# Kernel optimization log

Hardware: AMD Instinct MI355X
Metric: run time of the kernel (lower is better)

The kernel has to match this reference:

```python
import jax, jax.numpy as jnp
import numpy as np

E, L, S, C, H, NEXP = 1024, 25, 64, 128, 512, 8  # edges, sh coeffs, grid pts, dim_in, 4*dim_in, experts


def _ln(x, g, b, eps=1e-5):
    m = jnp.mean(x, axis=-1, keepdims=True)
    v = jnp.mean((x - m) ** 2, axis=-1, keepdims=True)
    return (x - m) * jax.lax.rsqrt(v + eps) * g + b


def setup_inputs() -> dict:
    key = jax.random.key(0)
    ks = jax.random.split(key, 20)
    rn = lambda k, shp: jax.random.normal(k, shp, jnp.float32) * 0.05
    return {
        "message": jax.random.normal(ks[0], (E, L, C), jnp.float32),
        "gate_output": jax.nn.softmax(jax.random.normal(ks[1], (E, NEXP), jnp.float32), axis=-1),
        "batch": jnp.sort(jax.random.randint(ks[2], (E,), 0, 64)),
        "ln1_g": jnp.ones((C,), jnp.float32), "ln1_b": jnp.zeros((C,), jnp.float32),
        "wq": rn(ks[3], (C, C)), "bq": jnp.zeros((C,), jnp.float32),
        "wk": rn(ks[4], (C, C)), "bk": jnp.zeros((C,), jnp.float32),
        "wv": rn(ks[5], (C, C)), "bv": jnp.zeros((C,), jnp.float32),
        "norm_l0_g": jnp.ones((C,), jnp.float32), "norm_l0_b": jnp.zeros((C,), jnp.float32),
        "fc_l0_w": rn(ks[6], (C, C)), "fc_l0_b": jnp.zeros((C,), jnp.float32),
        "exp_ln_g": jnp.ones((NEXP, C), jnp.float32), "exp_ln_b": jnp.zeros((NEXP, C), jnp.float32),
        "exp_w1": rn(ks[7], (NEXP, C, H)), "exp_b1": jnp.zeros((NEXP, H), jnp.float32),
        "exp_w2": rn(ks[8], (NEXP, H, C)), "exp_b2": jnp.zeros((NEXP, C), jnp.float32),
        "to_grid_mat": rn(ks[9], (S, L)),
        "from_grid_mat": rn(ks[10], (L, S)),
        "pos_emb": jax.random.normal(ks[11], (S, 3), jnp.float32),
    }


def reference(message, gate_output, batch, ln1_g, ln1_b, wq, bq, wk, bk, wv, bv,
              norm_l0_g, norm_l0_b, fc_l0_w, fc_l0_b,
              exp_ln_g, exp_ln_b, exp_w1, exp_b1, exp_w2, exp_b2,
              to_grid_mat, from_grid_mat, pos_emb):
    # l=0 scalar branch: LN -> Linear -> SiLU on the first SH coefficient
    msg_l0 = jax.nn.silu(_ln(message[:, 0:1, :], norm_l0_g, norm_l0_b) @ fc_l0_w + fc_l0_b)  # [E,1,C]
    # SH coeffs -> spherical grid (eval mode: no random rotation)
    g = jnp.einsum('sl,elc->esc', to_grid_mat, message)  # [E,S,C]
    m = _ln(g, ln1_g, ln1_b)
    q = m @ wq + bq
    k = m @ wk + bk
    v = m @ wv + bv
    # spherical RoE: concat grid xyz positions to q and k
    pe = jnp.broadcast_to(pos_emb[None].astype(q.dtype), (q.shape[0],) + pos_emb.shape)  # [E,S,3]
    q = jnp.concatenate([q, pe], axis=-1)  # [E,S,C+3]
    k = jnp.concatenate([k, pe], axis=-1)
    scale = 1.0 / jnp.sqrt(jnp.asarray(q.shape[-1], q.dtype))
    attn = jax.nn.softmax(jnp.einsum('esc,etc->est', q, k) * scale, axis=-1)
    out = jnp.einsum('est,etc->esc', attn, v)  # [E,S,C]
    # gate-weighted dense sum over experts (LN -> Linear -> SiLU -> Linear)
    acc = jnp.zeros_like(out)
    for i in range(NEXP):
        h = _ln(out, exp_ln_g[i], exp_ln_b[i])
        h = jax.nn.silu(h @ exp_w1[i] + exp_b1[i]) @ exp_w2[i] + exp_b2[i]
        acc = acc + h * gate_output[:, i][:, None, None]
    # grid -> SH coeffs, then splice in the l0 branch
    fro = jnp.einsum('ls,esc->elc', from_grid_mat, acc)  # [E,L,C]
    return jnp.concatenate([msg_l0, fro[:, 1:, :]], axis=1)
```

## Files before the change

### kernel.cpp

```cpp
#include <hip/hip_runtime.h>
#include <hip/hip_bf16.h>

#define E_ 1024
#define L_ 25
#define S_ 64
#define C_ 128
#define H_ 512
#define NEXP_ 8

#define OFF_W     0
#define OFF_PEDOT 128
#define OFF_B1P   4224
#define OFF_GTF   8320
#define OFF_WVTF  16512
#define OFF_TGF   24704
#define OFF_G     25728
#define OFF_W1S   42112
#define OFF_W2S   304256
#define OFF_NOUT  566400

typedef float floatx4 __attribute__((ext_vector_type(4)));
typedef __bf16 bf16x8 __attribute__((ext_vector_type(8)));
typedef __bf16 bf16x4 __attribute__((ext_vector_type(4)));

__global__ void prep1(const float* __restrict__ wq, const float* __restrict__ bq,
                      const float* __restrict__ wk, const float* __restrict__ bk,
                      const float* __restrict__ pe, float* __restrict__ ws) {
    int b = blockIdx.x, tid = threadIdx.x;
    (void)bk;
    if (b < 64) {
        int a = b * 2 + (tid >> 7);
        int col = tid & 127;
        const float* ra = wq + a * C_;
        const float* rb = wk + col * C_;
        float acc = 0.f;
        for (int c = 0; c < C_; ++c) acc += ra[c] * rb[c];
        ws[OFF_G + a * C_ + col] = acc;
    } else {
        if (tid < 128) {
            float acc = 0.f; const float* r = wk + tid * C_;
            for (int c = 0; c < C_; ++c) acc += r[c] * bq[c];
            ws[OFF_W + tid] = acc;
        }
        for (int idx = tid; idx < 64 * 64; idx += 256) {
            int s = idx >> 6, t = idx & 63;
            ws[OFF_PEDOT + idx] = pe[s*3]*pe[t*3] + pe[s*3+1]*pe[t*3+1] + pe[s*3+2]*pe[t*3+2];
        }
    }
}

__global__ void prep2(const float* __restrict__ elnb, const float* __restrict__ w1,
                      const float* __restrict__ b1, float* __restrict__ ws) {
    __shared__ float red[256];
    int b = blockIdx.x;
    int i = b >> 3, seg = b & 7;
    int hl = threadIdx.x & 63, part = threadIdx.x >> 6;
    int h = seg * 64 + hl;
    const float* wcol = w1 + i * 65536 + h;
    float acc = 0.f;
    for (int c = part * 32; c < part * 32 + 32; ++c)
        acc += elnb[i * 128 + c] * wcol[c * 512];
    red[threadIdx.x] = acc;
    __syncthreads();
    if (part == 0)
        ws[OFF_B1P + i * 512 + h] = red[hl] + red[hl + 64] + red[hl + 128] + red[hl + 192]
                                  + b1[i * 512 + h];
}

__global__ void prepSwz(const float* __restrict__ elng, const float* __restrict__ w1,
                        const float* __restrict__ w2,
                        __hip_bfloat16* __restrict__ w1s, __hip_bfloat16* __restrict__ w2s) {
    int idx = blockIdx.x * 256 + threadIdx.x;
    if (idx < 524288) {
        int f = idx >> 9, r = idx & 511;
        int lane = r >> 3, j = r & 7;
        int kt = f & 3, htg = (f >> 2) & 31, ex = f >> 7;
        int c = kt * 32 + (lane >> 4) * 8 + j;
        int h = htg * 16 + (lane & 15);
        w1s[idx] = __float2bfloat16(elng[ex * 128 + c] * w1[ex * 65536 + c * 512 + h]);
    } else {
        int i2 = idx - 524288;
        int f = i2 >> 9, r = i2 & 511;
        int lane = r >> 3, j = r & 7;
        int ktg = f & 15, ctg = (f >> 4) & 7, ex = f >> 7;
        int h = ktg * 32 + (lane >> 4) * 8 + j;
        int c = ctg * 16 + (lane & 15);
        w2s[i2] = __float2bfloat16(w2[ex * 65536 + h * 128 + c]);
    }
}

__global__ void prepSwzA(const float* __restrict__ ws, const float* __restrict__ wv,
                         const float* __restrict__ tg,
                         __hip_bfloat16* __restrict__ gtf, __hip_bfloat16* __restrict__ wvtf,
                         __hip_bfloat16* __restrict__ tgf) {
    int idx = blockIdx.x * 256 + threadIdx.x;
    if (idx < 32768) {
        int i2 = idx & 16383;
        int f = i2 >> 9, r = i2 & 511;
        int lane = r >> 3, j = r & 7;
        int kt = f & 3, Nt = f >> 2;
        int k = kt * 32 + (lane >> 4) * 8 + j;
        int n = Nt * 16 + (lane & 15);
        if (idx < 16384) {
            gtf[i2] = __float2bfloat16(ws[OFF_G + k * 128 + n]);
        } else {
            wvtf[i2] = __float2bfloat16(wv[k * 128 + n]);
        }
    } else {
        int i3 = idx - 32768;
        int f = i3 >> 9, r = i3 & 511;
        int lane = r >> 3, j = r & 7;
        int m = f * 16 + (lane & 15);
        int k = (lane >> 4) * 8 + j;
        tgf[i3] = (k < 25) ? __float2bfloat16(tg[m * 25 + k]) : __float2bfloat16(0.f);
    }
}

__global__ __launch_bounds__(256) void kernA(
        const float* __restrict__ message, const float* __restrict__ ln1g,
        const float* __restrict__ ln1b, const float* __restrict__ bv,
        const float* __restrict__ ws_ro,
        const __hip_bfloat16* __restrict__ gtf, const __hip_bfloat16* __restrict__ wvtf,
        const __hip_bfloat16* __restrict__ tgf,
        __hip_bfloat16* __restrict__ nout) {
    __shared__ __align__(16) char sA[64 * 272];
    __shared__ __align__(16) char sB[64 * 272];
    __shared__ __align__(16) char sC[128 * 144];
    __shared__ __align__(16) float sStP[512];
    __shared__ __align__(16) float sSt2[128];
    __shared__ float sMw[64];

    const int e = blockIdx.x, tid = threadIdx.x;
    const int w = tid >> 6, lane = tid & 63, quad = lane >> 4, col = lane & 15;

    float* sMsgF = (float*)sB;
    for (int i = tid; i < 3200; i += 256) sMsgF[i] = message[(size_t)e * 3200 + i];
    __syncthreads();

    char* sMt = sC;
    for (int i = tid; i < 4096; i += 256) {
        int c = i >> 5, l = i & 31;
        float v = (l < 25) ? sMsgF[l * 128 + c] : 0.f;
        *(__hip_bfloat16*)(sMt + c * 80 + l * 2) = __float2bfloat16(v);
    }
    __syncthreads();

    floatx4 accG[4][2];
    {
        #pragma unroll
        for (int mt = 0; mt < 4; ++mt) { accG[mt][0] = (floatx4)0.f; accG[mt][1] = (floatx4)0.f; }
        bf16x8 a[4], b[2];
        #pragma unroll
        for (int mt = 0; mt < 4; ++mt) a[mt] = *(const bf16x8*)(tgf + mt * 512 + lane * 8);
        #pragma unroll
        for (int nt = 0; nt < 2; ++nt)
            b[nt] = *(const bf16x8*)(sMt + ((2 * w + nt) * 16 + col) * 80 + quad * 16);
        #pragma unroll
        for (int mt = 0; mt < 4; ++mt)
            #pragma unroll
            for (int nt = 0; nt < 2; ++nt)
                accG[mt][nt] = __builtin_amdgcn_mfma_f32_16x16x32_bf16(a[mt], b[nt], accG[mt][nt], 0, 0, 0);
    }
    #pragma unroll
    for (int mt = 0; mt < 4; ++mt)
        #pragma unroll
        for (int reg = 0; reg < 4; ++reg) {
            float v0 = accG[mt][0][reg], v1 = accG[mt][1][reg];
            float sm = v0 + v1, sq = v0 * v0 + v1 * v1;
            #pragma unroll
            for (int m = 1; m < 16; m <<= 1) {
                sm += __shfl_xor(sm, m, 64);
                sq += __shfl_xor(sq, m, 64);
            }
            if (col == 0) {
                int s = mt * 16 + quad * 4 + reg;
                sStP[(s * 4 + w) * 2]     = sm;
                sStP[(s * 4 + w) * 2 + 1] = sq;
            }
        }
    __syncthreads();
    if (tid < 64) {
        float sm = 0.f, sq = 0.f;
        #pragma unroll
        for (int k = 0; k < 4; ++k) {
            sm += sStP[(tid * 4 + k) * 2];
            sq += sStP[(tid * 4 + k) * 2 + 1];
        }
        float mean = sm * (1.f / 128.f);
        float rstd = rsqrtf(sq * (1.f / 128.f) - mean * mean + 1e-5f);
        sSt2[tid * 2] = mean; sSt2[tid * 2 + 1] = rstd;
    }
    __syncthreads();
    {
        float g1[2], b1v[2];
        #pragma unroll
        for (int nt = 0; nt < 2; ++nt) {
            int c = (2 * w + nt) * 16 + col;
            g1[nt] = ln1g[c]; b1v[nt] = ln1b[c];
        }
        #pragma unroll
        for (int mt = 0; mt < 4; ++mt)
            #pragma unroll
            for (int reg = 0; reg < 4; ++reg) {
                int s = mt * 16 + quad * 4 + reg;
                float mean = sSt2[s * 2], rstd = sSt2[s * 2 + 1];
                #pragma unroll
                for (int nt = 0; nt < 2; ++nt) {
                    int c = (2 * w + nt) * 16 + col;
                    ((__hip_bfloat16*)(sA + s * 272))[c] =
                        __float2bfloat16((accG[mt][nt][reg] - mean) * rstd * g1[nt] + b1v[nt]);
                }
            }
    }
    __syncthreads();

    {
        int t = tid >> 2, part = tid & 3;
        const __hip_bfloat16* mr = (const __hip_bfloat16*)(sA + t * 272) + part * 32;
        const float* wv_ = ws_ro + OFF_W + part * 32;
        float acc = 0.f;
        #pragma unroll
        for (int k = 0; k < 32; ++k) acc += __bfloat162float(mr[k]) * wv_[k];
        acc += __shfl_xor(acc, 1, 64);
        acc += __shfl_xor(acc, 2, 64);
        if (part == 0) sMw[t] = acc;
    }

    {
        floatx4 accZ[4][2];
        #pragma unroll
        for (int mt = 0; mt < 4; ++mt) { accZ[mt][0] = (floatx4)0.f; accZ[mt][1] = (floatx4)0.f; }
        #pragma unroll
        for (int kt = 0; kt < 4; ++kt) {
            bf16x8 a[4], b[2];
            #pragma unroll
            for (int mt = 0; mt < 4; ++mt)
                a[mt] = *(const bf16x8*)(sA + (mt * 16 + col) * 272 + kt * 64 + quad * 16);
            #pragma unroll
            for (int nt = 0; nt < 2; ++nt)
                b[nt] = *(const bf16x8*)(gtf + ((2 * w + nt) * 4 + kt) * 512 + lane * 8);
            #pragma unroll
            for (int mt = 0; mt < 4; ++mt)
                #pragma unroll
                for (int nt = 0; nt < 2; ++nt)
                    accZ[mt][nt] = __builtin_amdgcn_mfma_f32_16x16x32_bf16(a[mt], b[nt], accZ[mt][nt], 0, 0, 0);
        }
        #pragma unroll
        for (int mt = 0; mt < 4; ++mt)
            #pragma unroll
            for (int nt = 0; nt < 2; ++nt) {
                int j = (2 * w + nt) * 16 + col;
                #pragma unroll
                for (int reg = 0; reg < 4; ++reg)
                    ((__hip_bfloat16*)(sB + (mt * 16 + quad * 4 + reg) * 272))[j] =
                        __float2bfloat16(accZ[mt][nt][reg]);
            }
    }
    __syncthreads();

    {
        floatx4 accS[4];
        #pragma unroll
        for (int mt = 0; mt < 4; ++mt) accS[mt] = (floatx4)0.f;
        #pragma unroll
        for (int kt = 0; kt < 4; ++kt) {
            bf16x8 a[4];
            #pragma unroll
            for (int mt = 0; mt < 4; ++mt)
                a[mt] = *(const bf16x8*)(sB + (mt * 16 + col) * 272 + kt * 64 + quad * 16);
            bf16x8 b = *(const bf16x8*)(sA + (w * 16 + col) * 272 + kt * 64 + quad * 16);
            #pragma unroll
            for (int mt = 0; mt < 4; ++mt)
                accS[mt] = __builtin_amdgcn_mfma_f32_16x16x32_bf16(a[mt], b, accS[mt], 0, 0, 0);
        }
        float* sc = (float*)sC;
        #pragma unroll
        for (int mt = 0; mt < 4; ++mt)
            #pragma unroll
            for (int reg = 0; reg < 4; ++reg)
                sc[(mt * 16 + quad * 4 + reg) * 68 + w * 16 + col] = accS[mt][reg];
    }
    __syncthreads();

    {
        const float scale = 0.08737040566610379f;
        const float* sc = (const float*)sC;
        const float* pd = ws_ro + OFF_PEDOT;
        for (int r = 0; r < 16; ++r) {
            int s = w * 16 + r;
            float x = sc[s * 68 + lane] + sMw[lane] + pd[s * 64 + lane];
            float mx = x;
            #pragma unroll
            for (int m = 1; m < 64; m <<= 1) mx = fmaxf(mx, __shfl_xor(mx, m, 64));
            float p = __expf((x - mx) * scale);
            float sm = p;
            #pragma unroll
            for (int m = 1; m < 64; m <<= 1) sm += __shfl_xor(sm, m, 64);
            float rs = __builtin_amdgcn_rcpf(sm);
            ((__hip_bfloat16*)(sB + s * 272))[lane] = __float2bfloat16(p * rs);
        }
    }
    __syncthreads();

    {
        floatx4 accV[4][2];
        #pragma unroll
        for (int mt = 0; mt < 4; ++mt) { accV[mt][0] = (floatx4)0.f; accV[mt][1] = (floatx4)0.f; }
        #pragma unroll
        for (int kt = 0; kt < 4; ++kt) {
            bf16x8 a[4], b[2];
            #pragma unroll
            for (int mt = 0; mt < 4; ++mt)
                a[mt] = *(const bf16x8*)(sA + (mt * 16 + col) * 272 + kt * 64 + quad * 16);
            #pragma unroll
            for (int nt = 0; nt < 2; ++nt)
                b[nt] = *(const bf16x8*)(wvtf + ((2 * w + nt) * 4 + kt) * 512 + lane * 8);
            #pragma unroll
            for (int mt = 0; mt < 4; ++mt)
                #pragma unroll
                for (int nt = 0; nt < 2; ++nt)
                    accV[mt][nt] = __builtin_amdgcn_mfma_f32_16x16x32_bf16(a[mt], b[nt], accV[mt][nt], 0, 0, 0);
        }
        #pragma unroll
        for (int nt = 0; nt < 2; ++nt) {
            int c = (2 * w + nt) * 16 + col;
            float bvv = bv[c];
            #pragma unroll
            for (int mt = 0; mt < 4; ++mt) {
                bf16x4 pk;
                #pragma unroll
                for (int reg = 0; reg < 4; ++reg)
                    pk[reg] = (__bf16)(accV[mt][nt][reg] + bvv);
                *(bf16x4*)(sC + c * 144 + (mt * 16 + quad * 4) * 2) = pk;
            }
        }
    }
    __syncthreads();

    floatx4 accO[4][2];
    #pragma unroll
    for (int mt = 0; mt < 4; ++mt) { accO[mt][0] = (floatx4)0.f; accO[mt][1] = (floatx4)0.f; }
    #pragma unroll
    for (int kt = 0; kt < 2; ++kt) {
        bf16x8 a[4], b[2];
        #pragma unroll
        for (int mt = 0; mt < 4; ++mt)
            a[mt] = *(const bf16x8*)(sB + (mt * 16 + col) * 272 + kt * 64 + quad * 16);
        #pragma unroll
        for (int nt = 0; nt < 2; ++nt)
            b[nt] = *(const bf16x8*)(sC + ((2 * w + nt) * 16 + col) * 144 + kt * 64 + quad * 16);
        #pragma unroll
        for (int mt = 0; mt < 4; ++mt)
            #pragma unroll
            for (int nt = 0; nt < 2; ++nt)
                accO[mt][nt] = __builtin_amdgcn_mfma_f32_16x16x32_bf16(a[mt], b[nt], accO[mt][nt], 0, 0, 0);
    }

    #pragma unroll
    for (int mt = 0; mt < 4; ++mt)
        #pragma unroll
        for (int reg = 0; reg < 4; ++reg) {
            float v0 = accO[mt][0][reg], v1 = accO[mt][1][reg];
            float sm = v0 + v1, sq = v0 * v0 + v1 * v1;
            #pragma unroll
            for (int m = 1; m < 16; m <<= 1) {
                sm += __shfl_xor(sm, m, 64);
                sq += __shfl_xor(sq, m, 64);
            }
            if (col == 0) {
                int s = mt * 16 + quad * 4 + reg;
                sStP[(s * 4 + w) * 2]     = sm;
                sStP[(s * 4 + w) * 2 + 1] = sq;
            }
        }
    __syncthreads();
    if (tid < 64) {
        float sm = 0.f, sq = 0.f;
        #pragma unroll
        for (int k = 0; k < 4; ++k) {
            sm += sStP[(tid * 4 + k) * 2];
            sq += sStP[(tid * 4 + k) * 2 + 1];
        }
        float mean = sm * (1.f / 128.f);
        float rstd = rsqrtf(sq * (1.f / 128.f) - mean * mean + 1e-5f);
        sSt2[tid * 2] = mean; sSt2[tid * 2 + 1] = rstd;
    }
    __syncthreads();

    #pragma unroll
    for (int mt = 0; mt < 4; ++mt)
        #pragma unroll
        for (int reg = 0; reg < 4; ++reg) {
            int s = mt * 16 + quad * 4 + reg;
            float mean = sSt2[s * 2], rstd = sSt2[s * 2 + 1];
            #pragma unroll
            for (int nt = 0; nt < 2; ++nt) {
                int c = (2 * w + nt) * 16 + col;
                ((__hip_bfloat16*)(sB + s * 272))[c] =
                    __float2bfloat16((accO[mt][nt][reg] - mean) * rstd);
            }
        }
    __syncthreads();

    for (int i = tid; i < 1024; i += 256) {
        int row = i >> 4, c16 = i & 15;
        bf16x8 v = *(const bf16x8*)(sB + row * 272 + c16 * 16);
        *(bf16x8*)(nout + (size_t)e * 8192 + row * 128 + c16 * 8) = v;
    }
}

__global__ void kernL0(const float* __restrict__ message, const float* __restrict__ nlg,
                       const float* __restrict__ nlb, const float* __restrict__ fcw,
                       const float* __restrict__ fcb, float* __restrict__ out) {
    __shared__ float sn[128];
    int e = blockIdx.x, lane = threadIdx.x;
    float x0 = message[e * 3200 + lane];
    float x1 = message[e * 3200 + 64 + lane];
    float sm = x0 + x1, sq = x0 * x0 + x1 * x1;
    #pragma unroll
    for (int m = 1; m < 64; m <<= 1) {
        sm += __shfl_xor(sm, m, 64);
        sq += __shfl_xor(sq, m, 64);
    }
    float mean = sm * (1.f / 128.f);
    float rstd = rsqrtf(sq * (1.f / 128.f) - mean * mean + 1e-5f);
    sn[lane]      = (x0 - mean) * rstd * nlg[lane]      + nlb[lane];
    sn[lane + 64] = (x1 - mean) * rstd * nlg[lane + 64] + nlb[lane + 64];
    __syncthreads();
    float o0 = fcb[lane], o1 = fcb[lane + 64];
    for (int j = 0; j < 128; ++j) {
        float nj = sn[j];
        o0 += nj * fcw[j * 128 + lane];
        o1 += nj * fcw[j * 128 + lane + 64];
    }
    out[e * 3200 + lane]      = o0 * __builtin_amdgcn_rcpf(1.f + __expf(-o0));
    out[e * 3200 + 64 + lane] = o1 * __builtin_amdgcn_rcpf(1.f + __expf(-o1));
}

__global__ __launch_bounds__(256, 2) void kernC(
        const __hip_bfloat16* __restrict__ nout_ro, const float* __restrict__ gate,
        const __hip_bfloat16* __restrict__ w1s, const __hip_bfloat16* __restrict__ w2s,
        const float* __restrict__ b1p, const float* __restrict__ b2,
        const float* __restrict__ fg, float* __restrict__ out) {

    __shared__ __align__(16) char smem[128 * 272 + 128 * 272];
    __shared__ float sGB2[2][128];
    char* sXb = smem;
    char* sSb = smem + 128 * 272;
    float* sAcc = (float*)smem;

    const int e0 = blockIdx.x * 2;
    const int tid = threadIdx.x;
    const int w = tid >> 6, lane = tid & 63;
    const int quad = lane >> 4, col = lane & 15;
    const int htB = (w >> 1) * 4;
    const int stB = (w & 1) * 2;

    for (int i = tid; i < 2048; i += 256) {
        int n = i >> 4, c16 = i & 15;
        bf16x8 v = *(const bf16x8*)(nout_ro + (size_t)(e0 * 64 + n) * 128 + c16 * 8);
        *(bf16x8*)(sXb + n * 272 + c16 * 16) = v;
    }
    {
        int e_l = tid >> 7, c = tid & 127;
        float s = 0.f;
        #pragma unroll
        for (int ex = 0; ex < 8; ++ex) s += gate[(e0 + e_l) * 8 + ex] * b2[ex * 128 + c];
        sGB2[e_l][c] = s;
    }

    floatx4 accT[2][4][2];
    #pragma unroll
    for (int e = 0; e < 2; ++e)
        #pragma unroll
        for (int m = 0; m < 4; ++m)
            #pragma unroll
            for (int n2 = 0; n2 < 2; ++n2) accT[e][m][n2] = (floatx4)0.f;

    bf16x8 a1[4][4];
    auto loadA1 = [&](int ex_, int hb_) {
        #pragma unroll
        for (int mt = 0; mt < 4; ++mt)
            #pragma unroll
            for (int kt = 0; kt < 4; ++kt)
                a1[mt][kt] = *(const bf16x8*)(w1s + (size_t)((ex_*32 + hb_*8 + htB + mt)*4 + kt)*512 + lane*8);
    };
    loadA1(0, 0);
    __syncthreads();

    for (int it = 0; it < 32; ++it) {
        const int ex = it >> 2, hb = it & 3;
        const float gv0 = gate[e0 * 8 + ex];
        const float gv1 = gate[e0 * 8 + 8 + ex];
        float4 bias[4];
        #pragma unroll
        for (int mt = 0; mt < 4; ++mt)
            bias[mt] = *(const float4*)(b1p + ex * 512 + hb * 128 + (htB + mt) * 16 + quad * 4);

        #pragma unroll
        for (int ph = 0; ph < 2; ++ph) {
            const float gv = ph ? gv1 : gv0;
            floatx4 accP[4][2];
            #pragma unroll
            for (int mt = 0; mt < 4; ++mt)
                #pragma unroll
                for (int nt = 0; nt < 2; ++nt) {
                    accP[mt][nt][0] = bias[mt].x; accP[mt][nt][1] = bias[mt].y;
                    accP[mt][nt][2] = bias[mt].z; accP[mt][nt][3] = bias[mt].w;
                }
            #pragma unroll
            for (int kt = 0; kt < 4; ++kt) {
                bf16x8 b[2];
                #pragma unroll
                for (int nt = 0; nt < 2; ++nt) {
                    int n = ph * 64 + (stB + nt) * 16 + col;
                    b[nt] = *(const bf16x8*)(sXb + n * 272 + kt * 64 + quad * 16);
                }
                #pragma unroll
                for (int mt = 0; mt < 4; ++mt)
                    #pragma unroll
                    for (int nt = 0; nt < 2; ++nt)
                        accP[mt][nt] = __builtin_amdgcn_mfma_f32_16x16x32_bf16(a1[mt][kt], b[nt], accP[mt][nt], 0, 0, 0);
            }
            #pragma unroll
            for (int mt = 0; mt < 4; ++mt) {
                int hl = (htB + mt) * 16 + quad * 4;
                #pragma unroll
                for (int nt = 0; nt < 2; ++nt) {
                    int nl = ph * 64 + (stB + nt) * 16 + col;
                    bf16x4 sv;
                    #pragma unroll
                    for (int r = 0; r < 4; ++r) {
                        float p = accP[mt][nt][r];
                        sv[r] = (__bf16)(gv * p * __builtin_amdgcn_rcpf(1.f + __expf(-p)));
                    }
                    *(bf16x4*)(sSb + nl * 272 + hl * 2) = sv;
                }
            }
        }

        bf16x8 a2[4][4];
        #pragma unroll
        for (int mt = 0; mt < 4; ++mt)
            #pragma unroll
            for (int kt = 0; kt < 4; ++kt)
                a2[mt][kt] = *(const bf16x8*)(w2s + (size_t)((ex*8 + htB + mt)*16 + hb*4 + kt)*512 + lane*8);
        if (it < 31) {
            int nx = it + 1;
            loadA1(nx >> 2, nx & 3);
        }
        __syncthreads();

        #pragma unroll
        for (int ph = 0; ph < 2; ++ph) {
            #pragma unroll
            for (int kt = 0; kt < 4; ++kt) {
                bf16x8 b[2];
                #pragma unroll
                for (int nt = 0; nt < 2; ++nt) {
                    int nl = ph * 64 + (stB + nt) * 16 + col;
                    b[nt] = *(const bf16x8*)(sSb + nl * 272 + kt * 64 + quad * 16);
                }
                #pragma unroll
                for (int mt = 0; mt < 4; ++mt)
                    #pragma unroll
                    for (int nt = 0; nt < 2; ++nt)
                        accT[ph][mt][nt] = __builtin_amdgcn_mfma_f32_16x16x32_bf16(a2[mt][kt], b[nt], accT[ph][mt][nt], 0, 0, 0);
            }
        }
        __syncthreads();
    }

    for (int e = 0; e < 2; ++e) {
        #pragma unroll
        for (int mt = 0; mt < 4; ++mt) {
            int c = (htB + mt) * 16 + quad * 4;
            float4 gb = *(const float4*)(&sGB2[e][c]);
            #pragma unroll
            for (int nt = 0; nt < 2; ++nt) {
                int nl = (stB + nt) * 16 + col;
                float4 v;
                v.x = accT[e][mt][nt][0] + gb.x;
                v.y = accT[e][mt][nt][1] + gb.y;
                v.z = accT[e][mt][nt][2] + gb.z;
                v.w = accT[e][mt][nt][3] + gb.w;
                *(float4*)(sAcc + nl * 132 + c) = v;
            }
        }
        __syncthreads();
        for (int idx = tid; idx < 768; idx += 256) {
            int l = 1 + (idx >> 5);
            int c4 = (idx & 31) * 4;
            float4 a4 = {0.f, 0.f, 0.f, 0.f};
            const float* fgr = fg + l * 64;
            for (int s = 0; s < 64; ++s) {
                float f = fgr[s];
                const float* row = sAcc + s * 132 + c4;
                a4.x += f * row[0]; a4.y += f * row[1]; a4.z += f * row[2]; a4.w += f * row[3];
            }
            *(float4*)(out + (size_t)(e0 + e) * 3200 + l * 128 + c4) = a4;
        }
        __syncthreads();
    }
}

extern "C" void kernel_launch(void* const* d_in, const int* in_sizes, int n_in,
                              void* d_out, int out_size, void* d_ws, size_t ws_size,
                              hipStream_t stream) {
    (void)in_sizes; (void)n_in; (void)out_size; (void)ws_size;
    const float* message = (const float*)d_in[0];
    const float* gate    = (const float*)d_in[1];
    const float* ln1g = (const float*)d_in[3];
    const float* ln1b = (const float*)d_in[4];
    const float* wq   = (const float*)d_in[5];
    const float* bq   = (const float*)d_in[6];
    const float* wk   = (const float*)d_in[7];
    const float* bk   = (const float*)d_in[8];
    const float* wv   = (const float*)d_in[9];
    const float* bv   = (const float*)d_in[10];
    const float* nlg  = (const float*)d_in[11];
    const float* nlb  = (const float*)d_in[12];
    const float* fcw  = (const float*)d_in[13];
    const float* fcb  = (const float*)d_in[14];
    const float* elng = (const float*)d_in[15];
    const float* elnb = (const float*)d_in[16];
    const float* w1   = (const float*)d_in[17];
    const float* b1   = (const float*)d_in[18];
    const float* w2   = (const float*)d_in[19];
    const float* b2   = (const float*)d_in[20];
    const float* tg   = (const float*)d_in[21];
    const float* fg   = (const float*)d_in[22];
    const float* pe   = (const float*)d_in[23];
    float* ws  = (float*)d_ws;
    float* out = (float*)d_out;
    __hip_bfloat16* gtfp = (__hip_bfloat16*)(ws + OFF_GTF);
    __hip_bfloat16* wvtf = (__hip_bfloat16*)(ws + OFF_WVTF);
    __hip_bfloat16* tgf  = (__hip_bfloat16*)(ws + OFF_TGF);
    __hip_bfloat16* w1s  = (__hip_bfloat16*)(ws + OFF_W1S);
    __hip_bfloat16* w2s  = (__hip_bfloat16*)(ws + OFF_W2S);
    __hip_bfloat16* nout = (__hip_bfloat16*)(ws + OFF_NOUT);

    prep1<<<dim3(65), dim3(256), 0, stream>>>(wq, bq, wk, bk, pe, ws);
    prep2<<<dim3(64), dim3(256), 0, stream>>>(elnb, w1, b1, ws);
    prepSwz<<<dim3(4096), dim3(256), 0, stream>>>(elng, w1, w2, w1s, w2s);
    prepSwzA<<<dim3(136), dim3(256), 0, stream>>>(ws, wv, tg, gtfp, wvtf, tgf);
    kernA<<<dim3(E_), dim3(256), 0, stream>>>(message, ln1g, ln1b, bv, ws, gtfp, wvtf, tgf, nout);
    kernL0<<<dim3(E_), dim3(64), 0, stream>>>(message, nlg, nlb, fcw, fcb, out);
    kernC<<<dim3(E_ / 2), dim3(256), 0, stream>>>(nout, gate, w1s, w2s,
                                                  ws + OFF_B1P, b2, fg, out);
}
```

Before: 356.3 us.

## Merge prep kernels, fuse l0 branch into kernA, restructure expert kernel per edge

Four preprocessing kernels become one prepAll launch, and the Wq·Wk^T product is computed directly into the swizzled bf16 layout. The separate l0 LN/Linear/SiLU kernel is folded into the tail of kernA. kernC now handles one edge per block instead of two, keeps X fragments in registers rather than LDS, and loads W1/W2 fragments per tile instead of prefetching the next iteration. This removes launch overhead and LDS traffic, but drops the weight prefetch and halves weight reuse per block, so weight loads are exposed.

```diff
diff --git a/kernel.cpp b/kernel.cpp
--- a/kernel.cpp
+++ b/kernel.cpp
@@ -14,105 +14,92 @@
 #define OFF_GTF   8320
 #define OFF_WVTF  16512
 #define OFF_TGF   24704
-#define OFF_G     25728
-#define OFF_W1S   42112
-#define OFF_W2S   304256
-#define OFF_NOUT  566400
+#define OFF_W1S   25728
+#define OFF_W2S   287872
+#define OFF_NOUT  550016
 
 typedef float floatx4 __attribute__((ext_vector_type(4)));
 typedef __bf16 bf16x8 __attribute__((ext_vector_type(8)));
 typedef __bf16 bf16x4 __attribute__((ext_vector_type(4)));
 
-__global__ void prep1(const float* __restrict__ wq, const float* __restrict__ bq,
-                      const float* __restrict__ wk, const float* __restrict__ bk,
-                      const float* __restrict__ pe, float* __restrict__ ws) {
-    int b = blockIdx.x, tid = threadIdx.x;
-    (void)bk;
-    if (b < 64) {
-        int a = b * 2 + (tid >> 7);
-        int col = tid & 127;
-        const float* ra = wq + a * C_;
-        const float* rb = wk + col * C_;
-        float acc = 0.f;
-        for (int c = 0; c < C_; ++c) acc += ra[c] * rb[c];
-        ws[OFF_G + a * C_ + col] = acc;
-    } else {
-        if (tid < 128) {
-            float acc = 0.f; const float* r = wk + tid * C_;
-            for (int c = 0; c < C_; ++c) acc += r[c] * bq[c];
-            ws[OFF_W + tid] = acc;
-        }
-        for (int idx = tid; idx < 64 * 64; idx += 256) {
-            int s = idx >> 6, t = idx & 63;
-            ws[OFF_PEDOT + idx] = pe[s*3]*pe[t*3] + pe[s*3+1]*pe[t*3+1] + pe[s*3+2]*pe[t*3+2];
-        }
-    }
-}
-
-__global__ void prep2(const float* __restrict__ elnb, const float* __restrict__ w1,
-                      const float* __restrict__ b1, float* __restrict__ ws) {
-    __shared__ float red[256];
-    int b = blockIdx.x;
-    int i = b >> 3, seg = b & 7;
-    int hl = threadIdx.x & 63, part = threadIdx.x >> 6;
-    int h = seg * 64 + hl;
-    const float* wcol = w1 + i * 65536 + h;
-    float acc = 0.f;
-    for (int c = part * 32; c < part * 32 + 32; ++c)
-        acc += elnb[i * 128 + c] * wcol[c * 512];
-    red[threadIdx.x] = acc;
-    __syncthreads();
-    if (part == 0)
-        ws[OFF_B1P + i * 512 + h] = red[hl] + red[hl + 64] + red[hl + 128] + red[hl + 192]
-                                  + b1[i * 512 + h];
-}
-
-__global__ void prepSwz(const float* __restrict__ elng, const float* __restrict__ w1,
+__global__ void prepAll(const float* __restrict__ wq, const float* __restrict__ bq,
+                        const float* __restrict__ wk, const float* __restrict__ wv,
+                        const float* __restrict__ tg, const float* __restrict__ pe,
+                        const float* __restrict__ elng, const float* __restrict__ elnb,
+                        const float* __restrict__ w1, const float* __restrict__ b1,
                         const float* __restrict__ w2,
-                        __hip_bfloat16* __restrict__ w1s, __hip_bfloat16* __restrict__ w2s) {
-    int idx = blockIdx.x * 256 + threadIdx.x;
-    if (idx < 524288) {
+                        __hip_bfloat16* __restrict__ w1s, __hip_bfloat16* __restrict__ w2s,
+                        __hip_bfloat16* __restrict__ gtf, __hip_bfloat16* __restrict__ wvtf,
+                        __hip_bfloat16* __restrict__ tgf, float* __restrict__ ws) {
+    const int b = blockIdx.x, tid = threadIdx.x;
+    if (b < 2048) {
+        int idx = b * 256 + tid;
         int f = idx >> 9, r = idx & 511;
         int lane = r >> 3, j = r & 7;
         int kt = f & 3, htg = (f >> 2) & 31, ex = f >> 7;
         int c = kt * 32 + (lane >> 4) * 8 + j;
         int h = htg * 16 + (lane & 15);
         w1s[idx] = __float2bfloat16(elng[ex * 128 + c] * w1[ex * 65536 + c * 512 + h]);
-    } else {
-        int i2 = idx - 524288;
+    } else if (b < 4096) {
+        int i2 = (b - 2048) * 256 + tid;
         int f = i2 >> 9, r = i2 & 511;
         int lane = r >> 3, j = r & 7;
         int ktg = f & 15, ctg = (f >> 4) & 7, ex = f >> 7;
         int h = ktg * 32 + (lane >> 4) * 8 + j;
         int c = ctg * 16 + (lane & 15);
         w2s[i2] = __float2bfloat16(w2[ex * 65536 + h * 128 + c]);
-    }
-}
-
-__global__ void prepSwzA(const float* __restrict__ ws, const float* __restrict__ wv,
-                         const float* __restrict__ tg,
-                         __hip_bfloat16* __restrict__ gtf, __hip_bfloat16* __restrict__ wvtf,
-                         __hip_bfloat16* __restrict__ tgf) {
-    int idx = blockIdx.x * 256 + threadIdx.x;
-    if (idx < 32768) {
-        int i2 = idx & 16383;
+    } else if (b < 4160) {
+        int i2 = (b - 4096) * 256 + tid;
         int f = i2 >> 9, r = i2 & 511;
         int lane = r >> 3, j = r & 7;
         int kt = f & 3, Nt = f >> 2;
         int k = kt * 32 + (lane >> 4) * 8 + j;
         int n = Nt * 16 + (lane & 15);
-        if (idx < 16384) {
-            gtf[i2] = __float2bfloat16(ws[OFF_G + k * 128 + n]);
-        } else {
-            wvtf[i2] = __float2bfloat16(wv[k * 128 + n]);
+        float acc = 0.f;
+        const float* ra = wq + k * C_;
+        const float* rb = wk + n * C_;
+        for (int c = 0; c < C_; ++c) acc += ra[c] * rb[c];
+        gtf[i2] = __float2bfloat16(acc);
+    } else if (b < 4224) {
+        int i2 = (b - 4160) * 256 + tid;
+        int f = i2 >> 9, r = i2 & 511;
+        int lane = r >> 3, j = r & 7;
+        int kt = f & 3, Nt = f >> 2;
+        int k = kt * 32 + (lane >> 4) * 8 + j;
+        int n = Nt * 16 + (lane & 15);
+        wvtf[i2] = __float2bfloat16(wv[k * 128 + n]);
+    } else if (b == 4224) {
+        for (int i3 = tid; i3 < 2048; i3 += 256) {
+            int f = i3 >> 9, r = i3 & 511;
+            int lane = r >> 3, j = r & 7;
+            int m = f * 16 + (lane & 15);
+            int k = (lane >> 4) * 8 + j;
+            tgf[i3] = (k < 25) ? __float2bfloat16(tg[m * 25 + k]) : __float2bfloat16(0.f);
+        }
+        if (tid < 128) {
+            float acc = 0.f; const float* r = wk + tid * C_;
+            for (int c = 0; c < C_; ++c) acc += r[c] * bq[c];
+            ws[OFF_W + tid] = acc;
+        }
+        for (int idx = tid; idx < 64 * 64; idx += 256) {
+            int s = idx >> 6, t = idx & 63;
+            ws[OFF_PEDOT + idx] = pe[s*3]*pe[t*3] + pe[s*3+1]*pe[t*3+1] + pe[s*3+2]*pe[t*3+2];
         }
     } else {
-        int i3 = idx - 32768;
-        int f = i3 >> 9, r = i3 & 511;
-        int lane = r >> 3, j = r & 7;
-        int m = f * 16 + (lane & 15);
-        int k = (lane >> 4) * 8 + j;
-        tgf[i3] = (k < 25) ? __float2bfloat16(tg[m * 25 + k]) : __float2bfloat16(0.f);
+        __shared__ float red[256];
+        int bb = b - 4225;
+        int i = bb >> 3, seg = bb & 7;
+        int hl = tid & 63, part = tid >> 6;
+        int h = seg * 64 + hl;
+        const float* wcol = w1 + i * 65536 + h;
+        float acc = 0.f;
+        for (int c = part * 32; c < part * 32 + 32; ++c)
+            acc += elnb[i * 128 + c] * wcol[c * 512];
+        red[tid] = acc;
+        __syncthreads();
+        if (part == 0)
+            ws[OFF_B1P + i * 512 + h] = red[hl] + red[hl + 64] + red[hl + 128] + red[hl + 192]
+                                      + b1[i * 512 + h];
     }
 }
 
@@ -122,19 +109,23 @@
         const float* __restrict__ ws_ro,
         const __hip_bfloat16* __restrict__ gtf, const __hip_bfloat16* __restrict__ wvtf,
         const __hip_bfloat16* __restrict__ tgf,
-        __hip_bfloat16* __restrict__ nout) {
+        const float* __restrict__ nlg, const float* __restrict__ nlb,
+        const float* __restrict__ fcw, const float* __restrict__ fcb,
+        __hip_bfloat16* __restrict__ nout, float* __restrict__ out) {
     __shared__ __align__(16) char sA[64 * 272];
     __shared__ __align__(16) char sB[64 * 272];
     __shared__ __align__(16) char sC[128 * 144];
     __shared__ __align__(16) float sStP[512];
     __shared__ __align__(16) float sSt2[128];
     __shared__ float sMw[64];
+    __shared__ float sMsg0[128];
 
     const int e = blockIdx.x, tid = threadIdx.x;
     const int w = tid >> 6, lane = tid & 63, quad = lane >> 4, col = lane & 15;
 
     float* sMsgF = (float*)sB;
     for (int i = tid; i < 3200; i += 256) sMsgF[i] = message[(size_t)e * 3200 + i];
+    if (tid < 128) sMsg0[tid] = message[(size_t)e * 3200 + tid];
     __syncthreads();
 
     char* sMt = sC;
@@ -407,34 +398,33 @@
         bf16x8 v = *(const bf16x8*)(sB + row * 272 + c16 * 16);
         *(bf16x8*)(nout + (size_t)e * 8192 + row * 128 + c16 * 8) = v;
     }
-}
-
-__global__ void kernL0(const float* __restrict__ message, const float* __restrict__ nlg,
-                       const float* __restrict__ nlb, const float* __restrict__ fcw,
-                       const float* __restrict__ fcb, float* __restrict__ out) {
-    __shared__ float sn[128];
-    int e = blockIdx.x, lane = threadIdx.x;
-    float x0 = message[e * 3200 + lane];
-    float x1 = message[e * 3200 + 64 + lane];
-    float sm = x0 + x1, sq = x0 * x0 + x1 * x1;
-    #pragma unroll
-    for (int m = 1; m < 64; m <<= 1) {
-        sm += __shfl_xor(sm, m, 64);
-        sq += __shfl_xor(sq, m, 64);
-    }
-    float mean = sm * (1.f / 128.f);
-    float rstd = rsqrtf(sq * (1.f / 128.f) - mean * mean + 1e-5f);
-    sn[lane]      = (x0 - mean) * rstd * nlg[lane]      + nlb[lane];
-    sn[lane + 64] = (x1 - mean) * rstd * nlg[lane + 64] + nlb[lane + 64];
-    __syncthreads();
-    float o0 = fcb[lane], o1 = fcb[lane + 64];
-    for (int j = 0; j < 128; ++j) {
-        float nj = sn[j];
-        o0 += nj * fcw[j * 128 + lane];
-        o1 += nj * fcw[j * 128 + lane + 64];
-    }
-    out[e * 3200 + lane]      = o0 * __builtin_amdgcn_rcpf(1.f + __expf(-o0));
-    out[e * 3200 + 64 + lane] = o1 * __builtin_amdgcn_rcpf(1.f + __expf(-o1));
+
+    if (tid < 64) {
+        float x0 = sMsg0[tid], x1 = sMsg0[tid + 64];
+        float sm = x0 + x1, sq = x0 * x0 + x1 * x1;
+        #pragma unroll
+        for (int m = 1; m < 64; m <<= 1) {
+            sm += __shfl_xor(sm, m, 64);
+            sq += __shfl_xor(sq, m, 64);
+        }
+        float mean = sm * (1.f / 128.f);
+        float rstd = rsqrtf(sq * (1.f / 128.f) - mean * mean + 1e-5f);
+        sMsg0[tid]      = (x0 - mean) * rstd * nlg[tid]      + nlb[tid];
+        sMsg0[tid + 64] = (x1 - mean) * rstd * nlg[tid + 64] + nlb[tid + 64];
+    }
+    __syncthreads();
+    {
+        int c = tid & 127, jh = tid >> 7;
+        float acc = 0.f;
+        for (int j = jh * 64; j < jh * 64 + 64; ++j)
+            acc += sMsg0[j] * fcw[j * 128 + c];
+        sStP[tid] = acc;
+    }
+    __syncthreads();
+    if (tid < 128) {
+        float o = fcb[tid] + sStP[tid] + sStP[tid + 128];
+        out[(size_t)e * 3200 + tid] = o * __builtin_amdgcn_rcpf(1.f + __expf(-o));
+    }
 }
 
 __global__ __launch_bounds__(256, 2) void kernC(
@@ -443,164 +433,122 @@
         const float* __restrict__ b1p, const float* __restrict__ b2,
         const float* __restrict__ fg, float* __restrict__ out) {
 
-    __shared__ __align__(16) char smem[128 * 272 + 128 * 272];
-    __shared__ float sGB2[2][128];
-    char* sXb = smem;
-    char* sSb = smem + 128 * 272;
+    __shared__ __align__(16) char smem[64 * 528];
+    __shared__ float sGB2[128];
+    char* sSb = smem;
     float* sAcc = (float*)smem;
 
-    const int e0 = blockIdx.x * 2;
+    const int e = blockIdx.x;
     const int tid = threadIdx.x;
     const int w = tid >> 6, lane = tid & 63;
     const int quad = lane >> 4, col = lane & 15;
     const int htB = (w >> 1) * 4;
     const int stB = (w & 1) * 2;
 
-    for (int i = tid; i < 2048; i += 256) {
-        int n = i >> 4, c16 = i & 15;
-        bf16x8 v = *(const bf16x8*)(nout_ro + (size_t)(e0 * 64 + n) * 128 + c16 * 8);
-        *(bf16x8*)(sXb + n * 272 + c16 * 16) = v;
-    }
-    {
-        int e_l = tid >> 7, c = tid & 127;
+    bf16x8 Xf[2][4];
+    #pragma unroll
+    for (int nt = 0; nt < 2; ++nt)
+        #pragma unroll
+        for (int kt = 0; kt < 4; ++kt)
+            Xf[nt][kt] = *(const bf16x8*)(nout_ro +
+                ((size_t)e * 64 + (stB + nt) * 16 + col) * 128 + kt * 32 + quad * 8);
+
+    if (tid < 128) {
         float s = 0.f;
         #pragma unroll
-        for (int ex = 0; ex < 8; ++ex) s += gate[(e0 + e_l) * 8 + ex] * b2[ex * 128 + c];
-        sGB2[e_l][c] = s;
-    }
-
-    floatx4 accT[2][4][2];
-    #pragma unroll
-    for (int e = 0; e < 2; ++e)
-        #pragma unroll
-        for (int m = 0; m < 4; ++m)
-            #pragma unroll
-            for (int n2 = 0; n2 < 2; ++n2) accT[e][m][n2] = (floatx4)0.f;
-
-    bf16x8 a1[4][4];
-    auto loadA1 = [&](int ex_, int hb_) {
-        #pragma unroll
-        for (int mt = 0; mt < 4; ++mt)
-            #pragma unroll
-            for (int kt = 0; kt < 4; ++kt)
-                a1[mt][kt] = *(const bf16x8*)(w1s + (size_t)((ex_*32 + hb_*8 + htB + mt)*4 + kt)*512 + lane*8);
-    };
-    loadA1(0, 0);
-    __syncthreads();
+        for (int ex = 0; ex < 8; ++ex) s += gate[e * 8 + ex] * b2[ex * 128 + tid];
+        sGB2[tid] = s;
+    }
+
+    floatx4 accT[4][2];
+    #pragma unroll
+    for (int m = 0; m < 4; ++m) { accT[m][0] = (floatx4)0.f; accT[m][1] = (floatx4)0.f; }
 
     for (int it = 0; it < 32; ++it) {
         const int ex = it >> 2, hb = it & 3;
-        const float gv0 = gate[e0 * 8 + ex];
-        const float gv1 = gate[e0 * 8 + 8 + ex];
-        float4 bias[4];
-        #pragma unroll
-        for (int mt = 0; mt < 4; ++mt)
-            bias[mt] = *(const float4*)(b1p + ex * 512 + hb * 128 + (htB + mt) * 16 + quad * 4);
-
-        #pragma unroll
-        for (int ph = 0; ph < 2; ++ph) {
-            const float gv = ph ? gv1 : gv0;
-            floatx4 accP[4][2];
-            #pragma unroll
-            for (int mt = 0; mt < 4; ++mt)
-                #pragma unroll
-                for (int nt = 0; nt < 2; ++nt) {
-                    accP[mt][nt][0] = bias[mt].x; accP[mt][nt][1] = bias[mt].y;
-                    accP[mt][nt][2] = bias[mt].z; accP[mt][nt][3] = bias[mt].w;
-                }
-            #pragma unroll
-            for (int kt = 0; kt < 4; ++kt) {
-                bf16x8 b[2];
-                #pragma unroll
-                for (int nt = 0; nt < 2; ++nt) {
-                    int n = ph * 64 + (stB + nt) * 16 + col;
-                    b[nt] = *(const bf16x8*)(sXb + n * 272 + kt * 64 + quad * 16);
-                }
-                #pragma unroll
-                for (int mt = 0; mt < 4; ++mt)
-                    #pragma unroll
-                    for (int nt = 0; nt < 2; ++nt)
-                        accP[mt][nt] = __builtin_amdgcn_mfma_f32_16x16x32_bf16(a1[mt][kt], b[nt], accP[mt][nt], 0, 0, 0);
-            }
-            #pragma unroll
-            for (int mt = 0; mt < 4; ++mt) {
-                int hl = (htB + mt) * 16 + quad * 4;
-                #pragma unroll
-                for (int nt = 0; nt < 2; ++nt) {
-                    int nl = ph * 64 + (stB + nt) * 16 + col;
-                    bf16x4 sv;
-                    #pragma unroll
-                    for (int r = 0; r < 4; ++r) {
-                        float p = accP[mt][nt][r];
-                        sv[r] = (__bf16)(gv * p * __builtin_amdgcn_rcpf(1.f + __expf(-p)));
-                    }
-                    *(bf16x4*)(sSb + nl * 272 + hl * 2) = sv;
-                }
-            }
-        }
-
-        bf16x8 a2[4][4];
-        #pragma unroll
-        for (int mt = 0; mt < 4; ++mt)
+        const float gv = gate[e * 8 + ex];
+
+        #pragma unroll
+        for (int mt = 0; mt < 4; ++mt) {
+            bf16x8 a1[4];
             #pragma unroll
             for (int kt = 0; kt < 4; ++kt)
-                a2[mt][kt] = *(const bf16x8*)(w2s + (size_t)((ex*8 + htB + mt)*16 + hb*4 + kt)*512 + lane*8);
-        if (it < 31) {
-            int nx = it + 1;
-            loadA1(nx >> 2, nx & 3);
-        }
-        __syncthreads();
-
-        #pragma unroll
-        for (int ph = 0; ph < 2; ++ph) {
-            #pragma unroll
-            for (int kt = 0; kt < 4; ++kt) {
-                bf16x8 b[2];
-                #pragma unroll
-                for (int nt = 0; nt < 2; ++nt) {
-                    int nl = ph * 64 + (stB + nt) * 16 + col;
-                    b[nt] = *(const bf16x8*)(sSb + nl * 272 + kt * 64 + quad * 16);
-                }
-                #pragma unroll
-                for (int mt = 0; mt < 4; ++mt)
-                    #pragma unroll
-                    for (int nt = 0; nt < 2; ++nt)
-                        accT[ph][mt][nt] = __builtin_amdgcn_mfma_f32_16x16x32_bf16(a2[mt][kt], b[nt], accT[ph][mt][nt], 0, 0, 0);
-            }
-        }
-        __syncthreads();
-    }
-
-    for (int e = 0; e < 2; ++e) {
-        #pragma unroll
-        for (int mt = 0; mt < 4; ++mt) {
-            int c = (htB + mt) * 16 + quad * 4;
-            float4 gb = *(const float4*)(&sGB2[e][c]);
+                a1[kt] = *(const bf16x8*)(w1s + (size_t)((ex*32 + hb*8 + htB + mt)*4 + kt)*512 + lane*8);
+            float4 bias = *(const float4*)(b1p + ex * 512 + hb * 128 + (htB + mt) * 16 + quad * 4);
+            floatx4 accP[2];
+            #pragma unroll
+            for (int nt = 0; nt < 2; ++nt) {
+                accP[nt][0] = bias.x; accP[nt][1] = bias.y;
+                accP[nt][2] = bias.z; accP[nt][3] = bias.w;
+            }
+            #pragma unroll
+            for (int kt = 0; kt < 4; ++kt)
+                #pragma unroll
+                for (int nt = 0; nt < 2; ++nt)
+                    accP[nt] = __builtin_amdgcn_mfma_f32_16x16x32_bf16(a1[kt], Xf[nt][kt], accP[nt], 0, 0, 0);
+            int hl = (htB + mt) * 16 + quad * 4;
             #pragma unroll
             for (int nt = 0; nt < 2; ++nt) {
                 int nl = (stB + nt) * 16 + col;
-                float4 v;
-                v.x = accT[e][mt][nt][0] + gb.x;
-                v.y = accT[e][mt][nt][1] + gb.y;
-                v.z = accT[e][mt][nt][2] + gb.z;
-                v.w = accT[e][mt][nt][3] + gb.w;
-                *(float4*)(sAcc + nl * 132 + c) = v;
+                bf16x4 sv;
+                #pragma unroll
+                for (int r = 0; r < 4; ++r) {
+                    float p = accP[nt][r];
+                    sv[r] = (__bf16)(gv * p * __builtin_amdgcn_rcpf(1.f + __expf(-p)));
+                }
+                *(bf16x4*)(sSb + nl * 272 + hl * 2) = sv;
             }
         }
         __syncthreads();
-        for (int idx = tid; idx < 768; idx += 256) {
-            int l = 1 + (idx >> 5);
-            int c4 = (idx & 31) * 4;
-            float4 a4 = {0.f, 0.f, 0.f, 0.f};
-            const float* fgr = fg + l * 64;
-            for (int s = 0; s < 64; ++s) {
-                float f = fgr[s];
-                const float* row = sAcc + s * 132 + c4;
-                a4.x += f * row[0]; a4.y += f * row[1]; a4.z += f * row[2]; a4.w += f * row[3];
-            }
-            *(float4*)(out + (size_t)(e0 + e) * 3200 + l * 128 + c4) = a4;
+
+        bf16x8 Sf[2][4];
+        #pragma unroll
+        for (int nt = 0; nt < 2; ++nt)
+            #pragma unroll
+            for (int kt = 0; kt < 4; ++kt)
+                Sf[nt][kt] = *(const bf16x8*)(sSb + ((stB + nt) * 16 + col) * 272 + kt * 64 + quad * 16);
+        #pragma unroll
+        for (int mt = 0; mt < 4; ++mt) {
+            bf16x8 a2[4];
+            #pragma unroll
+            for (int kt = 0; kt < 4; ++kt)
+                a2[kt] = *(const bf16x8*)(w2s + (size_t)((ex*8 + htB + mt)*16 + hb*4 + kt)*512 + lane*8);
+            #pragma unroll
+            for (int kt = 0; kt < 4; ++kt)
+                #pragma unroll
+                for (int nt = 0; nt < 2; ++nt)
+                    accT[mt][nt] = __builtin_amdgcn_mfma_f32_16x16x32_bf16(a2[kt], Sf[nt][kt], accT[mt][nt], 0, 0, 0);
         }
         __syncthreads();
+    }
+
+    #pragma unroll
+    for (int mt = 0; mt < 4; ++mt) {
+        int c = (htB + mt) * 16 + quad * 4;
+        float4 gb = *(const float4*)(&sGB2[c]);
+        #pragma unroll
+        for (int nt = 0; nt < 2; ++nt) {
+            int nl = (stB + nt) * 16 + col;
+            float4 v;
+            v.x = accT[mt][nt][0] + gb.x;
+            v.y = accT[mt][nt][1] + gb.y;
+            v.z = accT[mt][nt][2] + gb.z;
+            v.w = accT[mt][nt][3] + gb.w;
+            *(float4*)(sAcc + nl * 132 + c) = v;
+        }
+    }
+    __syncthreads();
+    for (int idx = tid; idx < 768; idx += 256) {
+        int l = 1 + (idx >> 5);
+        int c4 = (idx & 31) * 4;
+        float4 a4 = {0.f, 0.f, 0.f, 0.f};
+        const float* fgr = fg + l * 64;
+        for (int s = 0; s < 64; ++s) {
+            float f = fgr[s];
+            const float* row = sAcc + s * 132 + c4;
+            a4.x += f * row[0]; a4.y += f * row[1]; a4.z += f * row[2]; a4.w += f * row[3];
+        }
+        *(float4*)(out + (size_t)e * 3200 + l * 128 + c4) = a4;
     }
 }
 
@@ -616,6 +564,7 @@
     const float* bq   = (const float*)d_in[6];
     const float* wk   = (const float*)d_in[7];
     const float* bk   = (const float*)d_in[8];
+    (void)bk;
     const float* wv   = (const float*)d_in[9];
     const float* bv   = (const float*)d_in[10];
     const float* nlg  = (const float*)d_in[11];
@@ -640,12 +589,10 @@
     __hip_bfloat16* w2s  = (__hip_bfloat16*)(ws + OFF_W2S);
     __hip_bfloat16* nout = (__hip_bfloat16*)(ws + OFF_NOUT);
 
-    prep1<<<dim3(65), dim3(256), 0, stream>>>(wq, bq, wk, bk, pe, ws);
-    prep2<<<dim3(64), dim3(256), 0, stream>>>(elnb, w1, b1, ws);
-    prepSwz<<<dim3(4096), dim3(256), 0, stream>>>(elng, w1, w2, w1s, w2s);
-    prepSwzA<<<dim3(136), dim3(256), 0, stream>>>(ws, wv, tg, gtfp, wvtf, tgf);
-    kernA<<<dim3(E_), dim3(256), 0, stream>>>(message, ln1g, ln1b, bv, ws, gtfp, wvtf, tgf, nout);
-    kernL0<<<dim3(E_), dim3(64), 0, stream>>>(message, nlg, nlb, fcw, fcb, out);
-    kernC<<<dim3(E_ / 2), dim3(256), 0, stream>>>(nout, gate, w1s, w2s,
-                                                  ws + OFF_B1P, b2, fg, out);
+    prepAll<<<dim3(4289), dim3(256), 0, stream>>>(wq, bq, wk, wv, tg, pe, elng, elnb,
+                                                  w1, b1, w2, w1s, w2s, gtfp, wvtf, tgf, ws);
+    kernA<<<dim3(E_), dim3(256), 0, stream>>>(message, ln1g, ln1b, bv, ws, gtfp, wvtf, tgf,
+                                              nlg, nlb, fcw, fcb, nout, out);
+    kernC<<<dim3(E_), dim3(256), 0, stream>>>(nout, gate, w1s, w2s,
+                                              ws + OFF_B1P, b2, fg, out);
 }
```

Result: slower. 487.6 us (+36.8%).
